# Optimization experiments

Measured on AMD Instinct MI355X. Metric: run time of the kernel, lower is better.

## Reference

```python
import jax, jax.numpy as jnp
import numpy as np

IN_DIM = 256
OUT_DIM = 256


def setup_inputs() -> dict:
    key = jax.random.key(0)
    k1, k2, k3, k4 = jax.random.split(key, 4)
    B, N = 8, 2048
    X = jax.random.normal(k1, (B, N, IN_DIM), dtype=jnp.float32)
    adj = jax.random.uniform(k2, (B, N, N), dtype=jnp.float32)
    # nn.Linear(input_dim, output_dim): W is [out, in], bias [out]
    bound = 1.0 / np.sqrt(IN_DIM)
    W = jax.random.uniform(k3, (OUT_DIM, IN_DIM), minval=-bound, maxval=bound, dtype=jnp.float32)
    b = jax.random.uniform(k4, (OUT_DIM,), minval=-bound, maxval=bound, dtype=jnp.float32)
    return {"X": X, "adj": adj, "W": W, "b": b}


def reference(X, adj, W, b):
    N = adj.shape[-1]
    # adj_hat = adj + I
    adj_hat = adj + jnp.eye(N, dtype=adj.dtype)
    # D^{-1/2} A_hat D^{-1/2}: diag matmuls are just row/col scaling
    d = jnp.sum(adj_hat, axis=-1) ** -0.5  # [B, N]
    adj_norm = d[..., :, None] * adj_hat * d[..., None, :]
    # aggregate then linear + relu
    H = jnp.matmul(adj_norm, X)  # [B, N, F_in]
    out = jnp.einsum('bnf,of->bno', H, W) + b
    return jax.nn.relu(out)
```

## Files before the change

kernel.cpp:

```cpp
#include <hip/hip_runtime.h>
#include <stdint.h>

typedef __attribute__((ext_vector_type(8))) short bf16x8;
typedef __attribute__((ext_vector_type(4))) float f32x4;
typedef unsigned short u16;

constexpr int NN = 2048, NF = 256;

__device__ inline u16 f2bf(float f) {
  uint32_t u = __builtin_bit_cast(uint32_t, f);
  uint32_t r = (u + 0x7FFFu + ((u >> 16) & 1u)) >> 16;
  return (u16)r;
}
__device__ inline float bf2f(u16 h) {
  uint32_t u = ((uint32_t)h) << 16;
  return __builtin_bit_cast(float, u);
}

__device__ inline void gload_lds16(const void* g, void* l) {
  __builtin_amdgcn_global_load_lds(
      (const __attribute__((address_space(1))) uint32_t*)g,
      (__attribute__((address_space(3))) uint32_t*)l,
      16, 0, 0);
}

__global__ __launch_bounds__(256) void k_rowsum(const float* __restrict__ adj,
                                                u16* __restrict__ adjb,
                                                float* __restrict__ d,
                                                const float* __restrict__ W,
                                                u16* __restrict__ Wb) {
  if (blockIdx.x >= 16384) {
    int i = (blockIdx.x - 16384) * 256 + threadIdx.x;
    float4 v = ((const float4*)W)[i];
    ushort4 o;
    o.x = f2bf(v.x); o.y = f2bf(v.y); o.z = f2bf(v.z); o.w = f2bf(v.w);
    *(ushort4*)(Wb + (size_t)i * 4) = o;
    return;
  }
  int row = blockIdx.x;
  const float4* p = (const float4*)(adj + (size_t)row * NN);
  u16* ob = adjb + (size_t)row * NN;
  float s = 0.f;
#pragma unroll
  for (int c = 0; c < 2; ++c) {
    int idx = threadIdx.x + 256 * c;
    float4 v = p[idx];
    s += v.x + v.y + v.z + v.w;
    ushort4 o;
    o.x = f2bf(v.x); o.y = f2bf(v.y); o.z = f2bf(v.z); o.w = f2bf(v.w);
    *(ushort4*)(ob + (size_t)idx * 4) = o;
  }
#pragma unroll
  for (int off = 32; off > 0; off >>= 1) s += __shfl_down(s, off, 64);
  __shared__ float red[4];
  int lane = threadIdx.x & 63, w = threadIdx.x >> 6;
  if (lane == 0) red[w] = s;
  __syncthreads();
  if (threadIdx.x == 0) {
    float t = red[0] + red[1] + red[2] + red[3] + 1.0f;
    d[row] = 1.0f / sqrtf(t);
  }
}

__global__ __launch_bounds__(256) void k_xprep(const float* __restrict__ X,
                                               const float* __restrict__ d,
                                               u16* __restrict__ XpT) {
  int jt = blockIdx.x, ft = blockIdx.y, b = blockIdx.z;
  int j0 = jt * 64, f0 = ft * 64;
  __shared__ u16 T[64][66];
  int t = threadIdx.x;
#pragma unroll
  for (int s = 0; s < 4; ++s) {
    int q = s * 256 + t;
    int r = q >> 4, c4 = q & 15;
    int j = j0 + r;
    float dv = d[b * NN + j];
    float4 v = *(const float4*)(X + ((size_t)(b * NN + j)) * NF + f0 + c4 * 4);
    T[r][c4 * 4 + 0] = f2bf(v.x * dv);
    T[r][c4 * 4 + 1] = f2bf(v.y * dv);
    T[r][c4 * 4 + 2] = f2bf(v.z * dv);
    T[r][c4 * 4 + 3] = f2bf(v.w * dv);
  }
  __syncthreads();
#pragma unroll
  for (int s = 0; s < 4; ++s) {
    int q = s * 256 + t;
    int fr = q >> 4, c4 = q & 15;
    ushort4 o;
    o.x = T[c4 * 4 + 0][fr]; o.y = T[c4 * 4 + 1][fr];
    o.z = T[c4 * 4 + 2][fr]; o.w = T[c4 * 4 + 3][fr];
    *(ushort4*)(XpT + ((size_t)(b * NF + f0 + fr)) * NN + j0 + c4 * 4) = o;
  }
}

#define BBASE 24576

#define FUSED_STEP(K, ARB, H, AW, BW, VMC, IA, IB)                             \
  {                                                                            \
    if (IA) gload_lds16(a_src + (size_t)((K) + 2) * 32,                        \
                        smem + (AW) * 8192 + aw_dst);                          \
    if (IB) {                                                                  \
      gload_lds16(b_src0 + (size_t)((K) + 2) * 32,                            \
                  smem + BBASE + (BW) * 16384 + bw_dst0);                      \
      gload_lds16(b_src1 + (size_t)((K) + 2) * 32,                            \
                  smem + BBASE + (BW) * 16384 + bw_dst1);                      \
    }                                                                          \
    __builtin_amdgcn_sched_barrier(0);                                         \
    asm volatile("s_waitcnt vmcnt(" VMC ")" ::: "memory");                     \
    __builtin_amdgcn_sched_barrier(0);                                         \
    __builtin_amdgcn_s_barrier();                                              \
    __builtin_amdgcn_sched_barrier(0);                                         \
    const char* Ab = smem + (ARB) * 8192 + ((H) << 12);                        \
    const char* Bb = smem + BBASE + ((K) & 3) * 16384;                         \
    bf16x8 af0 = *(const bf16x8*)(Ab + aoff0);                                 \
    bf16x8 af1 = *(const bf16x8*)(Ab + aoff0 + 1024);                          \
    bf16x8 b0 = *(const bf16x8*)(Bb + boff0);                                  \
    bf16x8 b1 = *(const bf16x8*)(Bb + boff0 + 1024);                           \
    bf16x8 b2 = *(const bf16x8*)(Bb + boff0 + 2048);                           \
    bf16x8 b3 = *(const bf16x8*)(Bb + boff0 + 3072);                           \
    asm volatile("s_waitcnt lgkmcnt(0)" ::: "memory");                         \
    __builtin_amdgcn_sched_barrier(0);                                         \
    __builtin_amdgcn_s_setprio(1);                                             \
    acc[0][0] = __builtin_amdgcn_mfma_f32_16x16x32_bf16(af0, b0, acc[0][0], 0, 0, 0); \
    acc[0][1] = __builtin_amdgcn_mfma_f32_16x16x32_bf16(af0, b1, acc[0][1], 0, 0, 0); \
    acc[0][2] = __builtin_amdgcn_mfma_f32_16x16x32_bf16(af0, b2, acc[0][2], 0, 0, 0); \
    acc[0][3] = __builtin_amdgcn_mfma_f32_16x16x32_bf16(af0, b3, acc[0][3], 0, 0, 0); \
    acc[1][0] = __builtin_amdgcn_mfma_f32_16x16x32_bf16(af1, b0, acc[1][0], 0, 0, 0); \
    acc[1][1] = __builtin_amdgcn_mfma_f32_16x16x32_bf16(af1, b1, acc[1][1], 0, 0, 0); \
    acc[1][2] = __builtin_amdgcn_mfma_f32_16x16x32_bf16(af1, b2, acc[1][2], 0, 0, 0); \
    acc[1][3] = __builtin_amdgcn_mfma_f32_16x16x32_bf16(af1, b3, acc[1][3], 0, 0, 0); \
    __builtin_amdgcn_s_setprio(0);                                             \
    __builtin_amdgcn_sched_barrier(0);                                         \
  }

__global__ __launch_bounds__(512, 2) void k_fused(
    const u16* __restrict__ adjb, const u16* __restrict__ XpT,
    const float* __restrict__ dsc, const u16* __restrict__ Wb,
    const float* __restrict__ bias, float* __restrict__ out) {
  int flat = blockIdx.x;
  int b = flat & 7, mt = flat >> 3;
  int i0 = mt * 64;

  __shared__ __align__(16) char smem[90112];
  u16* Hs = (u16*)smem;

  int t = threadIdx.x;
  int lane = t & 63, w = t >> 6;
  int l15 = lane & 15, l4 = lane >> 4;
  int wr = w >> 2, wc = w & 3;

  const u16* adjbb = adjb + ((size_t)b * NN + i0) * NN;
  const u16* XpTb = XpT + (size_t)b * NF * NN;

  int sA = (w << 6) + lane;
  int uA = sA >> 8;
  int rA = (sA >> 2) & 63;
  int cA = sA & 3;
  const u16* a_src = adjbb + (size_t)rA * NN + uA * 32 +
                     ((cA ^ ((rA >> 1) & 3)) << 3);
  int aw_dst = w << 10;

  int n0s = sA >> 2, c0s = sA & 3;
  const u16* b_src0 = XpTb + (size_t)n0s * NN + ((c0s ^ ((n0s >> 1) & 3)) << 3);
  int s1 = 512 + sA;
  int n1s = s1 >> 2, c1s = s1 & 3;
  const u16* b_src1 = XpTb + (size_t)n1s * NN + ((c1s ^ ((n1s >> 1) & 3)) << 3);
  int bw_dst0 = w << 10;
  int bw_dst1 = 8192 + (w << 10);

  int swz = (l4 ^ ((l15 >> 1) & 3)) << 4;
  int aoff0 = (wr * 32 + l15) * 64 + swz;
  int boff0 = (wc * 64 + l15) * 64 + swz;

  f32x4 acc[2][4] = {};

  gload_lds16(a_src, smem + aw_dst);
  gload_lds16(b_src0, smem + BBASE + bw_dst0);
  gload_lds16(b_src1, smem + BBASE + bw_dst1);
  gload_lds16(b_src0 + 32, smem + BBASE + 16384 + bw_dst0);
  gload_lds16(b_src1 + 32, smem + BBASE + 16384 + bw_dst1);
  __builtin_amdgcn_sched_barrier(0);

  for (int kb = 0; kb < 60; kb += 12) {
    FUSED_STEP(kb + 0, 0, 0, 1, 2, "5", 1, 1)
    FUSED_STEP(kb + 1, 0, 1, 0, 3, "5", 0, 1)
    FUSED_STEP(kb + 2, 1, 0, 2, 0, "5", 1, 1)
    FUSED_STEP(kb + 3, 1, 1, 0, 1, "5", 0, 1)
    FUSED_STEP(kb + 4, 2, 0, 0, 2, "5", 1, 1)
    FUSED_STEP(kb + 5, 2, 1, 0, 3, "5", 0, 1)
    FUSED_STEP(kb + 6, 0, 0, 1, 0, "5", 1, 1)
    FUSED_STEP(kb + 7, 0, 1, 0, 1, "5", 0, 1)
    FUSED_STEP(kb + 8, 1, 0, 2, 2, "5", 1, 1)
    FUSED_STEP(kb + 9, 1, 1, 0, 3, "5", 0, 1)
    FUSED_STEP(kb + 10, 2, 0, 0, 0, "5", 1, 1)
    FUSED_STEP(kb + 11, 2, 1, 0, 1, "5", 0, 1)
  }
  FUSED_STEP(60, 0, 0, 1, 2, "5", 1, 1)
  FUSED_STEP(61, 0, 1, 0, 3, "5", 0, 1)
  FUSED_STEP(62, 1, 0, 0, 0, "2", 0, 0)
  FUSED_STEP(63, 1, 1, 0, 0, "0", 0, 0)

  __syncthreads();

  const float* db = dsc + b * NN;
#pragma unroll
  for (int mi = 0; mi < 2; ++mi) {
#pragma unroll
    for (int ni = 0; ni < 4; ++ni) {
      int f = wc * 64 + ni * 16 + l15;
      ushort4 xv = *(const ushort4*)(XpTb + (size_t)f * NN + i0 +
                                     wr * 32 + mi * 16 + l4 * 4);
#pragma unroll
      for (int qq = 0; qq < 4; ++qq) {
        int il = wr * 32 + mi * 16 + l4 * 4 + qq;
        float dv = db[i0 + il];
        float xpv = bf2f(((const u16*)&xv)[qq]);
        float hv = dv * (acc[mi][ni][qq] + xpv);
        Hs[il * 264 + f] = f2bf(hv);
      }
    }
  }
  __syncthreads();

  f32x4 acc2[2][4] = {};
#pragma unroll
  for (int kk = 0; kk < 256; kk += 32) {
    bf16x8 a2[2], b2[4];
#pragma unroll
    for (int mi = 0; mi < 2; ++mi) {
      int r = wr * 32 + mi * 16 + l15;
      a2[mi] = *(const bf16x8*)&Hs[r * 264 + kk + l4 * 8];
    }
#pragma unroll
    for (int ni = 0; ni < 4; ++ni) {
      int o = wc * 64 + ni * 16 + l15;
      b2[ni] = *(const bf16x8*)&Wb[(size_t)o * 256 + kk + l4 * 8];
    }
#pragma unroll
    for (int mi = 0; mi < 2; ++mi)
#pragma unroll
      for (int ni = 0; ni < 4; ++ni)
        acc2[mi][ni] = __builtin_amdgcn_mfma_f32_16x16x32_bf16(a2[mi], b2[ni],
                                                               acc2[mi][ni], 0, 0, 0);
  }

  float* outb = out + ((size_t)b * NN + i0) * NF;
#pragma unroll
  for (int mi = 0; mi < 2; ++mi) {
#pragma unroll
    for (int qq = 0; qq < 4; ++qq) {
      int il = wr * 32 + mi * 16 + l4 * 4 + qq;
#pragma unroll
      for (int ni = 0; ni < 4; ++ni) {
        int o = wc * 64 + ni * 16 + l15;
        float v = acc2[mi][ni][qq] + bias[o];
        outb[(size_t)il * NF + o] = fmaxf(v, 0.f);
      }
    }
  }
}

extern "C" void kernel_launch(void* const* d_in, const int* in_sizes, int n_in,
                              void* d_out, int out_size, void* d_ws, size_t ws_size,
                              hipStream_t stream) {
  const float* X    = (const float*)d_in[0];
  const float* adj  = (const float*)d_in[1];
  const float* W    = (const float*)d_in[2];
  const float* bias = (const float*)d_in[3];
  float* out = (float*)d_out;

  char* ws = (char*)d_ws;
  float* dsc  = (float*)(ws);
  u16*   Wb   = (u16*)(ws + 65536);
  u16*   XpT  = (u16*)(ws + 262144);
  u16*   adjb = (u16*)(ws + 262144 + 8388608);

  k_rowsum<<<dim3(16448), dim3(256), 0, stream>>>(adj, adjb, dsc, W, Wb);
  k_xprep<<<dim3(32, 4, 8), dim3(256), 0, stream>>>(X, dsc, XpT);
  k_fused<<<dim3(256), dim3(512), 0, stream>>>(adjb, XpT, dsc, Wb, bias, out);
}
```

Baseline: 75.68 us.

## Fuse adj fp32-to-bf16 conversion into the fused GEMM load pipeline

Removes the bf16 copy of the adjacency matrix written by the row-sum kernel. The fused kernel instead loads fp32 adj rows into registers, converts them to bf16 and stores them swizzled into LDS, with a reworked pipeline that pairs k-steps and prefetches adj several steps ahead. This removes one full 64MB write and its intermediate buffer, at the cost of register-staged loads, extra conversion ALU work in the main loop and more register pressure.

```diff
diff --git a/kernel.cpp b/kernel.cpp
--- a/kernel.cpp
+++ b/kernel.cpp
@@ -2,6 +2,7 @@
 #include <stdint.h>
 
 typedef __attribute__((ext_vector_type(8))) short bf16x8;
+typedef __attribute__((ext_vector_type(8))) unsigned short u16x8;
 typedef __attribute__((ext_vector_type(4))) float f32x4;
 typedef unsigned short u16;
 
@@ -25,7 +26,6 @@
 }
 
 __global__ __launch_bounds__(256) void k_rowsum(const float* __restrict__ adj,
-                                                u16* __restrict__ adjb,
                                                 float* __restrict__ d,
                                                 const float* __restrict__ W,
                                                 u16* __restrict__ Wb) {
@@ -39,16 +39,11 @@
   }
   int row = blockIdx.x;
   const float4* p = (const float4*)(adj + (size_t)row * NN);
-  u16* ob = adjb + (size_t)row * NN;
   float s = 0.f;
 #pragma unroll
   for (int c = 0; c < 2; ++c) {
-    int idx = threadIdx.x + 256 * c;
-    float4 v = p[idx];
+    float4 v = p[threadIdx.x + 256 * c];
     s += v.x + v.y + v.z + v.w;
-    ushort4 o;
-    o.x = f2bf(v.x); o.y = f2bf(v.y); o.z = f2bf(v.z); o.w = f2bf(v.w);
-    *(ushort4*)(ob + (size_t)idx * 4) = o;
   }
 #pragma unroll
   for (int off = 32; off > 0; off >>= 1) s += __shfl_down(s, off, 64);
@@ -95,29 +90,14 @@
 
 #define BBASE 24576
 
-#define FUSED_STEP(K, ARB, H, AW, BW, VMC, IA, IB)                             \
+#define MFMA8(AB, BB)                                                          \
   {                                                                            \
-    if (IA) gload_lds16(a_src + (size_t)((K) + 2) * 32,                        \
-                        smem + (AW) * 8192 + aw_dst);                          \
-    if (IB) {                                                                  \
-      gload_lds16(b_src0 + (size_t)((K) + 2) * 32,                            \
-                  smem + BBASE + (BW) * 16384 + bw_dst0);                      \
-      gload_lds16(b_src1 + (size_t)((K) + 2) * 32,                            \
-                  smem + BBASE + (BW) * 16384 + bw_dst1);                      \
-    }                                                                          \
-    __builtin_amdgcn_sched_barrier(0);                                         \
-    asm volatile("s_waitcnt vmcnt(" VMC ")" ::: "memory");                     \
-    __builtin_amdgcn_sched_barrier(0);                                         \
-    __builtin_amdgcn_s_barrier();                                              \
-    __builtin_amdgcn_sched_barrier(0);                                         \
-    const char* Ab = smem + (ARB) * 8192 + ((H) << 12);                        \
-    const char* Bb = smem + BBASE + ((K) & 3) * 16384;                         \
-    bf16x8 af0 = *(const bf16x8*)(Ab + aoff0);                                 \
-    bf16x8 af1 = *(const bf16x8*)(Ab + aoff0 + 1024);                          \
-    bf16x8 b0 = *(const bf16x8*)(Bb + boff0);                                  \
-    bf16x8 b1 = *(const bf16x8*)(Bb + boff0 + 1024);                           \
-    bf16x8 b2 = *(const bf16x8*)(Bb + boff0 + 2048);                           \
-    bf16x8 b3 = *(const bf16x8*)(Bb + boff0 + 3072);                           \
+    bf16x8 af0 = *(const bf16x8*)((AB) + aoff0);                               \
+    bf16x8 af1 = *(const bf16x8*)((AB) + aoff0 + 1024);                        \
+    bf16x8 b0 = *(const bf16x8*)((BB) + boff0);                                \
+    bf16x8 b1 = *(const bf16x8*)((BB) + boff0 + 1024);                         \
+    bf16x8 b2 = *(const bf16x8*)((BB) + boff0 + 2048);                         \
+    bf16x8 b3 = *(const bf16x8*)((BB) + boff0 + 3072);                         \
     asm volatile("s_waitcnt lgkmcnt(0)" ::: "memory");                         \
     __builtin_amdgcn_sched_barrier(0);                                         \
     __builtin_amdgcn_s_setprio(1);                                             \
@@ -130,11 +110,55 @@
     acc[1][2] = __builtin_amdgcn_mfma_f32_16x16x32_bf16(af1, b2, acc[1][2], 0, 0, 0); \
     acc[1][3] = __builtin_amdgcn_mfma_f32_16x16x32_bf16(af1, b3, acc[1][3], 0, 0, 0); \
     __builtin_amdgcn_s_setprio(0);                                             \
+  }
+
+#define PAIR(G, RG, WG, SN, SW, BR0, BR1, BW0, BW1, VMC0, VMC1, IA, WA, IB0, IB1) \
+  {                                                                            \
+                                                 \
+    if (IB0) {                                                                 \
+      gload_lds16(b_src0 + (size_t)(2 * (G) + 2) * 32,                         \
+                  smem + BBASE + (BW0) * 16384 + bw0);                         \
+      gload_lds16(b_src1 + (size_t)(2 * (G) + 2) * 32,                         \
+                  smem + BBASE + (BW0) * 16384 + bw1);                         \
+    }                                                                          \
+    if (IA) {                                                                  \
+      aN0[SN] = *(const float4*)(a_gsrc + (size_t)((G) + 4) * 64);             \
+      aN1[SN] = *(const float4*)(a_gsrc + (size_t)((G) + 4) * 64 + 4);         \
+    }                                                                          \
+    __builtin_amdgcn_sched_barrier(0);                                         \
+    asm volatile("s_waitcnt vmcnt(" VMC0 ") lgkmcnt(0)" ::: "memory");         \
+    __builtin_amdgcn_sched_barrier(0);                                         \
+    __builtin_amdgcn_s_barrier();                                              \
+    __builtin_amdgcn_sched_barrier(0);                                         \
+    MFMA8(smem + (RG) * 8192, smem + BBASE + (BR0) * 16384)                    \
+    __builtin_amdgcn_sched_barrier(0);                                         \
+    if (WA) {                                                                  \
+      float4 c0 = aN0[SW], c1 = aN1[SW];                                       \
+      u16x8 pk;                                                                \
+      pk[0] = f2bf(c0.x); pk[1] = f2bf(c0.y); pk[2] = f2bf(c0.z);              \
+      pk[3] = f2bf(c0.w); pk[4] = f2bf(c1.x); pk[5] = f2bf(c1.y);              \
+      pk[6] = f2bf(c1.z); pk[7] = f2bf(c1.w);                                  \
+      *(u16x8*)(smem + (WG) * 8192 + a_ldst) = pk;                             \
+    }                                                                          \
+    __builtin_amdgcn_sched_barrier(0);                                         \
+                                                \
+    if (IB1) {                                                                 \
+      gload_lds16(b_src0 + (size_t)(2 * (G) + 3) * 32,                         \
+                  smem + BBASE + (BW1) * 16384 + bw0);                         \
+      gload_lds16(b_src1 + (size_t)(2 * (G) + 3) * 32,                         \
+                  smem + BBASE + (BW1) * 16384 + bw1);                         \
+    }                                                                          \
+    __builtin_amdgcn_sched_barrier(0);                                         \
+    asm volatile("s_waitcnt vmcnt(" VMC1 ") lgkmcnt(0)" ::: "memory");         \
+    __builtin_amdgcn_sched_barrier(0);                                         \
+    __builtin_amdgcn_s_barrier();                                              \
+    __builtin_amdgcn_sched_barrier(0);                                         \
+    MFMA8(smem + (RG) * 8192 + 4096, smem + BBASE + (BR1) * 16384)             \
     __builtin_amdgcn_sched_barrier(0);                                         \
   }
 
 __global__ __launch_bounds__(512, 2) void k_fused(
-    const u16* __restrict__ adjb, const u16* __restrict__ XpT,
+    const float* __restrict__ adj, const u16* __restrict__ XpT,
     const float* __restrict__ dsc, const u16* __restrict__ Wb,
     const float* __restrict__ bias, float* __restrict__ out) {
   int flat = blockIdx.x;
@@ -149,56 +173,72 @@
   int l15 = lane & 15, l4 = lane >> 4;
   int wr = w >> 2, wc = w & 3;
 
-  const u16* adjbb = adjb + ((size_t)b * NN + i0) * NN;
+  const float* adjf = adj + ((size_t)b * NN + i0) * NN;
   const u16* XpTb = XpT + (size_t)b * NF * NN;
 
-  int sA = (w << 6) + lane;
-  int uA = sA >> 8;
-  int rA = (sA >> 2) & 63;
-  int cA = sA & 3;
-  const u16* a_src = adjbb + (size_t)rA * NN + uA * 32 +
-                     ((cA ^ ((rA >> 1) & 3)) << 3);
-  int aw_dst = w << 10;
-
-  int n0s = sA >> 2, c0s = sA & 3;
+  int rA = t >> 3, kc = t & 7;
+  const float* a_gsrc = adjf + (size_t)rA * NN + kc * 8;
+  int a_ldst = (kc >> 2) * 4096 + rA * 64 + (((kc & 3) ^ ((rA >> 1) & 3)) << 4);
+
+  int n0s = t >> 2, c0s = t & 3;
   const u16* b_src0 = XpTb + (size_t)n0s * NN + ((c0s ^ ((n0s >> 1) & 3)) << 3);
-  int s1 = 512 + sA;
+  int s1 = 512 + t;
   int n1s = s1 >> 2, c1s = s1 & 3;
   const u16* b_src1 = XpTb + (size_t)n1s * NN + ((c1s ^ ((n1s >> 1) & 3)) << 3);
-  int bw_dst0 = w << 10;
-  int bw_dst1 = 8192 + (w << 10);
+  int bw0 = w << 10;
+  int bw1 = 8192 + (w << 10);
 
   int swz = (l4 ^ ((l15 >> 1) & 3)) << 4;
-  int aoff0 = (wr * 32 + l15) * 64 + swz;
+  int aoff0 = wr * 2048 + l15 * 64 + swz;
   int boff0 = (wc * 64 + l15) * 64 + swz;
 
   f32x4 acc[2][4] = {};
-
-  gload_lds16(a_src, smem + aw_dst);
-  gload_lds16(b_src0, smem + BBASE + bw_dst0);
-  gload_lds16(b_src1, smem + BBASE + bw_dst1);
-  gload_lds16(b_src0 + 32, smem + BBASE + 16384 + bw_dst0);
-  gload_lds16(b_src1 + 32, smem + BBASE + 16384 + bw_dst1);
-  __builtin_amdgcn_sched_barrier(0);
-
-  for (int kb = 0; kb < 60; kb += 12) {
-    FUSED_STEP(kb + 0, 0, 0, 1, 2, "5", 1, 1)
-    FUSED_STEP(kb + 1, 0, 1, 0, 3, "5", 0, 1)
-    FUSED_STEP(kb + 2, 1, 0, 2, 0, "5", 1, 1)
-    FUSED_STEP(kb + 3, 1, 1, 0, 1, "5", 0, 1)
-    FUSED_STEP(kb + 4, 2, 0, 0, 2, "5", 1, 1)
-    FUSED_STEP(kb + 5, 2, 1, 0, 3, "5", 0, 1)
-    FUSED_STEP(kb + 6, 0, 0, 1, 0, "5", 1, 1)
-    FUSED_STEP(kb + 7, 0, 1, 0, 1, "5", 0, 1)
-    FUSED_STEP(kb + 8, 1, 0, 2, 2, "5", 1, 1)
-    FUSED_STEP(kb + 9, 1, 1, 0, 3, "5", 0, 1)
-    FUSED_STEP(kb + 10, 2, 0, 0, 0, "5", 1, 1)
-    FUSED_STEP(kb + 11, 2, 1, 0, 1, "5", 0, 1)
-  }
-  FUSED_STEP(60, 0, 0, 1, 2, "5", 1, 1)
-  FUSED_STEP(61, 0, 1, 0, 3, "5", 0, 1)
-  FUSED_STEP(62, 1, 0, 0, 0, "2", 0, 0)
-  FUSED_STEP(63, 1, 1, 0, 0, "0", 0, 0)
+  float4 aN0[3], aN1[3];
+
+  {
+    float4 p0a = *(const float4*)(a_gsrc);
+    float4 p0b = *(const float4*)(a_gsrc + 4);
+    float4 p1a = *(const float4*)(a_gsrc + 64);
+    float4 p1b = *(const float4*)(a_gsrc + 68);
+    __builtin_amdgcn_sched_barrier(0);
+    gload_lds16(b_src0, smem + BBASE + bw0);
+    gload_lds16(b_src1, smem + BBASE + bw1);
+    gload_lds16(b_src0 + 32, smem + BBASE + 16384 + bw0);
+    gload_lds16(b_src1 + 32, smem + BBASE + 16384 + bw1);
+    __builtin_amdgcn_sched_barrier(0);
+    aN0[1] = *(const float4*)(a_gsrc + 128);
+    aN1[1] = *(const float4*)(a_gsrc + 132);
+    aN0[2] = *(const float4*)(a_gsrc + 192);
+    aN1[2] = *(const float4*)(a_gsrc + 196);
+    __builtin_amdgcn_sched_barrier(0);
+    u16x8 pk;
+    pk[0] = f2bf(p0a.x); pk[1] = f2bf(p0a.y); pk[2] = f2bf(p0a.z);
+    pk[3] = f2bf(p0a.w); pk[4] = f2bf(p0b.x); pk[5] = f2bf(p0b.y);
+    pk[6] = f2bf(p0b.z); pk[7] = f2bf(p0b.w);
+    *(u16x8*)(smem + a_ldst) = pk;
+    pk[0] = f2bf(p1a.x); pk[1] = f2bf(p1a.y); pk[2] = f2bf(p1a.z);
+    pk[3] = f2bf(p1a.w); pk[4] = f2bf(p1b.x); pk[5] = f2bf(p1b.y);
+    pk[6] = f2bf(p1b.z); pk[7] = f2bf(p1b.w);
+    *(u16x8*)(smem + 8192 + a_ldst) = pk;
+    __builtin_amdgcn_sched_barrier(0);
+  }
+
+  for (int gb = 0; gb < 24; gb += 6) {
+    PAIR(gb + 0, 0, 2, 0, 1, 0, 1, 2, 3, "8", "6", 1, 1, 1, 1)
+    PAIR(gb + 1, 1, 0, 1, 2, 2, 3, 0, 1, "8", "6", 1, 1, 1, 1)
+    PAIR(gb + 2, 2, 1, 2, 0, 0, 1, 2, 3, "8", "6", 1, 1, 1, 1)
+    PAIR(gb + 3, 0, 2, 0, 1, 2, 3, 0, 1, "8", "6", 1, 1, 1, 1)
+    PAIR(gb + 4, 1, 0, 1, 2, 0, 1, 2, 3, "8", "6", 1, 1, 1, 1)
+    PAIR(gb + 5, 2, 1, 2, 0, 2, 3, 0, 1, "8", "6", 1, 1, 1, 1)
+  }
+  PAIR(24, 0, 2, 0, 1, 0, 1, 2, 3, "8", "6", 1, 1, 1, 1)
+  PAIR(25, 1, 0, 1, 2, 2, 3, 0, 1, "8", "6", 1, 1, 1, 1)
+  PAIR(26, 2, 1, 2, 0, 0, 1, 2, 3, "8", "6", 1, 1, 1, 1)
+  PAIR(27, 0, 2, 0, 1, 2, 3, 0, 1, "8", "6", 1, 1, 1, 1)
+  PAIR(28, 1, 0, 1, 2, 0, 1, 2, 3, "6", "4", 0, 1, 1, 1)
+  PAIR(29, 2, 1, 2, 0, 2, 3, 0, 1, "4", "4", 0, 1, 1, 1)
+  PAIR(30, 0, 2, 0, 1, 0, 1, 2, 3, "4", "4", 0, 0, 1, 1)
+  PAIR(31, 1, 0, 1, 2, 2, 3, 0, 1, "2", "0", 0, 0, 0, 0)
 
   __syncthreads();
 
@@ -270,12 +310,11 @@
   float* out = (float*)d_out;
 
   char* ws = (char*)d_ws;
-  float* dsc  = (float*)(ws);
-  u16*   Wb   = (u16*)(ws + 65536);
-  u16*   XpT  = (u16*)(ws + 262144);
-  u16*   adjb = (u16*)(ws + 262144 + 8388608);
-
-  k_rowsum<<<dim3(16448), dim3(256), 0, stream>>>(adj, adjb, dsc, W, Wb);
+  float* dsc = (float*)(ws);
+  u16*   Wb  = (u16*)(ws + 65536);
+  u16*   XpT = (u16*)(ws + 262144);
+
+  k_rowsum<<<dim3(16448), dim3(256), 0, stream>>>(adj, dsc, W, Wb);
   k_xprep<<<dim3(32, 4, 8), dim3(256), 0, stream>>>(X, dsc, XpT);
-  k_fused<<<dim3(256), dim3(512), 0, stream>>>(adjb, XpT, dsc, Wb, bias, out);
-}
+  k_fused<<<dim3(256), dim3(512), 0, stream>>>(adj, XpT, dsc, Wb, bias, out);
+}
```

New measurement: 73.14 us. 3.4% less time.
